# Optimization experiments

Hardware: AMD Instinct MI355X
Metric: run time of the kernel (lower is better)

Reference implementation:

```python
import jax, jax.numpy as jnp
import numpy as np

B, T, C, H = 2, 2048, 1024, 16
D = C // H  # head_dim = 64

def setup_inputs() -> dict:
    key = jax.random.key(0)
    ks = jax.random.split(key, 9)
    s = 1.0 / np.sqrt(C)
    return {
        "x": jax.random.normal(ks[0], (B, T, C), dtype=jnp.float32),
        "Wq": jax.random.uniform(ks[1], (C, C), jnp.float32, -s, s),
        "bq": jax.random.uniform(ks[2], (C,), jnp.float32, -s, s),
        "Wk": jax.random.uniform(ks[3], (C, C), jnp.float32, -s, s),
        "bk": jax.random.uniform(ks[4], (C,), jnp.float32, -s, s),
        "Wv": jax.random.uniform(ks[5], (C, C), jnp.float32, -s, s),
        "bv": jax.random.uniform(ks[6], (C,), jnp.float32, -s, s),
        "Wp": jax.random.uniform(ks[7], (C, C), jnp.float32, -s, s),
        "bp": jax.random.uniform(ks[8], (C,), jnp.float32, -s, s),
    }

def reference(x, Wq, bq, Wk, bk, Wv, bv, Wp, bp):
    # Linear layers: torch nn.Linear weight is [out,in], so x @ W.T + b
    q = x @ Wq.T + bq
    k = x @ Wk.T + bk
    v = x @ Wv.T + bv
    # [B,T,C] -> [B,H,T,D]
    q = q.reshape(B, T, H, D).transpose(0, 2, 1, 3)
    k = k.reshape(B, T, H, D).transpose(0, 2, 1, 3)
    v = v.reshape(B, T, H, D).transpose(0, 2, 1, 3)
    att = jnp.einsum("bhqd,bhkd->bhqk", q, k) / jnp.sqrt(jnp.float32(D))
    causal = jnp.tril(jnp.ones((T, T), dtype=bool))  # [T,T]
    att = jnp.where(causal, att, jnp.float32(-jnp.inf))
    att = jax.nn.softmax(att, axis=-1)
    out = jnp.einsum("bhqk,bhkd->bhqd", att, v)
    out = out.transpose(0, 2, 1, 3).reshape(B, T, C)
    return out @ Wp.T + bp
```

## Files before the change

kernel.cpp:

```cpp
#include <hip/hip_runtime.h>
#include <hip/hip_bf16.h>
#include <stdint.h>

typedef __bf16 bf16x8 __attribute__((ext_vector_type(8)));
typedef __bf16 bf16x4 __attribute__((ext_vector_type(4)));
typedef __bf16 bf16x2 __attribute__((ext_vector_type(2)));
typedef float  f32x4  __attribute__((ext_vector_type(4)));
typedef float  f32x16v __attribute__((ext_vector_type(16)));

#define MFMA16(A,B,Cc) __builtin_amdgcn_mfma_f32_16x16x32_bf16(A,B,Cc,0,0,0)
#define MFMA32(A,B,Cc) __builtin_amdgcn_mfma_f32_32x32x16_bf16(A,B,Cc,0,0,0)

__device__ inline unsigned pack2(float a, float b) {
  union { bf16x2 v; unsigned u; } t;
  t.v[0] = (__bf16)a; t.v[1] = (__bf16)b;
  return t.u;
}
__device__ inline bf16x8 frag4(unsigned w0, unsigned w1, unsigned w2, unsigned w3) {
  union { unsigned u[4]; bf16x8 v; } t;
  t.u[0] = w0; t.u[1] = w1; t.u[2] = w2; t.u[3] = w3;
  return t.v;
}

__device__ inline void pswap(unsigned& a, unsigned& b) {
#if __has_builtin(__builtin_amdgcn_permlane32_swap)
  auto r = __builtin_amdgcn_permlane32_swap(a, b, false, false);
  a = r[0]; b = r[1];
#else
  asm volatile("v_permlane32_swap_b32 %0, %1" : "+v"(a), "+v"(b));
#endif
}
__device__ inline float cross32_max(float v) {
  unsigned a = __builtin_bit_cast(unsigned, v), b = a;
  pswap(a, b);
  return fmaxf(__builtin_bit_cast(float, a), __builtin_bit_cast(float, b));
}
__device__ inline float cross32_sum(float v) {
  unsigned a = __builtin_bit_cast(unsigned, v), b = a;
  pswap(a, b);
  return __builtin_bit_cast(float, a) + __builtin_bit_cast(float, b);
}

__device__ inline void gl16(const __bf16* g, __bf16* l) {
  __builtin_amdgcn_global_load_lds(
      (const __attribute__((address_space(1))) void*)(uintptr_t)g,
      (__attribute__((address_space(3))) void*)(uintptr_t)l, 16, 0, 0);
}

__global__ __launch_bounds__(256) void conv_kernel(
    const float* __restrict__ x,
    const float* __restrict__ Wq, const float* __restrict__ Wk,
    const float* __restrict__ Wv, const float* __restrict__ Wp,
    __bf16* __restrict__ xb, __bf16* __restrict__ Wb)
{
  const int z = blockIdx.y;
  const float* src;
  __bf16* dst;
  int n4;
  if (z == 0) { src = x;  dst = xb; n4 = 1048576; }
  else {
    src = (z == 1) ? Wq : (z == 2) ? Wk : (z == 3) ? Wv : Wp;
    dst = Wb + (size_t)(z - 1) * 1048576;
    n4  = 262144;
  }
  const f32x4* s4 = (const f32x4*)src;
  for (int i = blockIdx.x * 256 + threadIdx.x; i < n4; i += gridDim.x * 256) {
    const f32x4 v = s4[i];
    bf16x4 o;
#pragma unroll
    for (int j = 0; j < 4; ++j) o[j] = (__bf16)v[j];
    *(bf16x4*)(dst + (size_t)i * 4) = o;
  }
}

__device__ inline void gemm_core(const __bf16* __restrict__ A,
                                 const __bf16* __restrict__ W,
                                 int m0, int n0,
                                 __bf16* As, __bf16* Bs,
                                 f32x4 (&acc)[4][4])
{
  const int tid = threadIdx.x, lane = tid & 63;
  const int wid = tid >> 6, wr = wid >> 1, wc = wid & 1;
  const int g = lane >> 4, cl = lane & 15;
  const int sr = tid >> 2, sk = (tid & 3) * 8;
  __bf16* AsW = As + (tid & 192) * 8;
  __bf16* BsW = Bs + (tid & 192) * 8;

  for (int k0 = 0; k0 < 1024; k0 += 32) {
    __syncthreads();
    gl16(A + (size_t)(m0 + sr)      * 1024 + k0 + sk, AsW);
    gl16(A + (size_t)(m0 + sr + 64) * 1024 + k0 + sk, AsW + 2048);
    gl16(W + (size_t)(n0 + sr)      * 1024 + k0 + sk, BsW);
    gl16(W + (size_t)(n0 + sr + 64) * 1024 + k0 + sk, BsW + 2048);
    __syncthreads();
    bf16x8 af[4], bfr[4];
#pragma unroll
    for (int m = 0; m < 4; ++m)
      af[m] = *(const bf16x8*)(As + (wr * 64 + m * 16 + cl) * 32 + g * 8);
#pragma unroll
    for (int n = 0; n < 4; ++n)
      bfr[n] = *(const bf16x8*)(Bs + (wc * 64 + n * 16 + cl) * 32 + g * 8);
#pragma unroll
    for (int m = 0; m < 4; ++m)
#pragma unroll
      for (int n = 0; n < 4; ++n)
        acc[m][n] = MFMA16(af[m], bfr[n], acc[m][n]);
  }
}

__global__ __launch_bounds__(256) void gemm_qkv128(
    const __bf16* __restrict__ xb, const __bf16* __restrict__ Wb,
    const float* __restrict__ bq, const float* __restrict__ bk,
    const float* __restrict__ bv,
    __bf16* __restrict__ Qw, __bf16* __restrict__ Kw, __bf16* __restrict__ Vw)
{
  __shared__ __align__(16) __bf16 As[128 * 32];
  __shared__ __align__(16) __bf16 Bs[128 * 32];

  const int orig = blockIdx.x;
  const int wg   = (orig & 7) * 96 + (orig >> 3);
  const int z    = wg >> 8;
  const int rem  = wg & 255;
  const int m0   = (rem >> 3) * 128;
  const int n0   = (rem & 7) * 128;

  const __bf16* W  = Wb + (size_t)z * 1048576;
  const float*  bi = (z == 0) ? bq : (z == 1) ? bk : bv;
  __bf16*       out = (z == 0) ? Qw : (z == 1) ? Kw : Vw;

  f32x4 acc[4][4] = {};
  gemm_core(xb, W, m0, n0, As, Bs, acc);

  const int lane = threadIdx.x & 63, wid = threadIdx.x >> 6;
  const int wr = wid >> 1, wc = wid & 1;
  const int g = lane >> 4, cl = lane & 15;

  float bvv[4];
#pragma unroll
  for (int n = 0; n < 4; ++n) bvv[n] = bi[n0 + wc * 64 + n * 16 + cl];

#pragma unroll
  for (int m = 0; m < 4; ++m)
#pragma unroll
    for (int n = 0; n < 4; ++n) {
      const int col = n0 + wc * 64 + n * 16 + cl;
      const int h = col >> 6, d = col & 63;
      if (z == 2) {
        const int row0 = m0 + wr * 64 + m * 16 + g * 4;
        const int b2 = row0 >> 11, t0 = row0 & 2047;
        bf16x4 v4;
#pragma unroll
        for (int j = 0; j < 4; ++j) v4[j] = (__bf16)(acc[m][n][j] + bvv[n]);
        *(bf16x4*)(out + (size_t)(b2 * 16 + h) * 131072 + (size_t)d * 2048 + t0) = v4;
      } else {
#pragma unroll
        for (int j = 0; j < 4; ++j) {
          const int row = m0 + wr * 64 + m * 16 + g * 4 + j;
          const int b2 = row >> 11, t = row & 2047;
          out[(size_t)(b2 * 16 + h) * 131072 + (size_t)t * 64 + d] =
              (__bf16)(acc[m][n][j] + bvv[n]);
        }
      }
    }
}

__global__ __launch_bounds__(256) void gemm_proj128(
    const __bf16* __restrict__ A, const __bf16* __restrict__ W,
    const float* __restrict__ bi, float* __restrict__ outp)
{
  __shared__ __align__(16) __bf16 As[128 * 32];
  __shared__ __align__(16) __bf16 Bs[128 * 32];

  const int orig = blockIdx.x;
  const int wg   = (orig & 7) * 32 + (orig >> 3);
  const int m0   = (wg >> 3) * 128;
  const int n0   = (wg & 7) * 128;

  f32x4 acc[4][4] = {};
  gemm_core(A, W, m0, n0, As, Bs, acc);

  const int lane = threadIdx.x & 63, wid = threadIdx.x >> 6;
  const int wr = wid >> 1, wc = wid & 1;
  const int g = lane >> 4, cl = lane & 15;

  float bvv[4];
#pragma unroll
  for (int n = 0; n < 4; ++n) bvv[n] = bi[n0 + wc * 64 + n * 16 + cl];
#pragma unroll
  for (int m = 0; m < 4; ++m)
#pragma unroll
    for (int n = 0; n < 4; ++n) {
      const int col = n0 + wc * 64 + n * 16 + cl;
#pragma unroll
      for (int j = 0; j < 4; ++j) {
        const int row = m0 + wr * 64 + m * 16 + g * 4 + j;
        outp[(size_t)row * 1024 + col] = acc[m][n][j] + bvv[n];
      }
    }
}

__device__ inline void attn_tile(
    const __bf16* __restrict__ Kb, const __bf16* __restrict__ vrow0,
    const __bf16* __restrict__ vrow1, const bf16x8 (&qf)[4],
    int kv0, bool diag, int l31, int hi,
    float& M, float& MS, float& L, f32x16v& o0, f32x16v& o1)
{
  const float SC = 0.18033688f;
  const float DT = 16.6f;

  const bf16x8 kf0 = *(const bf16x8*)(Kb + (kv0 + l31) * 64 +      hi * 8);
  const bf16x8 kf1 = *(const bf16x8*)(Kb + (kv0 + l31) * 64 + 16 + hi * 8);
  const bf16x8 kf2 = *(const bf16x8*)(Kb + (kv0 + l31) * 64 + 32 + hi * 8);
  const bf16x8 kf3 = *(const bf16x8*)(Kb + (kv0 + l31) * 64 + 48 + hi * 8);
  const bf16x8 va0 = *(const bf16x8*)(vrow0 + kv0 + hi * 8);
  const bf16x8 va1 = *(const bf16x8*)(vrow1 + kv0 + hi * 8);
  const bf16x8 va2 = *(const bf16x8*)(vrow0 + kv0 + 16 + hi * 8);
  const bf16x8 va3 = *(const bf16x8*)(vrow1 + kv0 + 16 + hi * 8);

  f32x16v s = {};
  s = MFMA32(kf0, qf[0], s);
  s = MFMA32(kf1, qf[1], s);
  s = MFMA32(kf2, qf[2], s);
  s = MFMA32(kf3, qf[3], s);

  if (diag) {
#pragma unroll
    for (int r = 0; r < 16; ++r) {
      const int kl = (r & 3) + 8 * (r >> 2) + 4 * hi;
      if (kl > l31) s[r] = -1e30f;
    }
  }
  float mt = fmaxf(s[0], s[1]);
#pragma unroll
  for (int r = 2; r < 16; ++r) mt = fmaxf(mt, s[r]);
  mt = cross32_max(mt);
  if (!__all(mt <= M + DT)) {
    const float Mn = fmaxf(M, mt);
    const float rs = exp2f((M - Mn) * SC);
    o0 *= rs; o1 *= rs; L *= rs; M = Mn; MS = M * SC;
  }
  float pr[16];
  float lt = 0.f;
#pragma unroll
  for (int r = 0; r < 16; ++r) {
    pr[r] = exp2f(__builtin_fmaf(s[r], SC, -MS));
    lt += pr[r];
  }
  L += cross32_sum(lt);

  unsigned c0 = pack2(pr[0],  pr[1]),  c1 = pack2(pr[2],  pr[3]);
  unsigned c2 = pack2(pr[4],  pr[5]),  c3 = pack2(pr[6],  pr[7]);
  unsigned c4 = pack2(pr[8],  pr[9]),  c5 = pack2(pr[10], pr[11]);
  unsigned c6 = pack2(pr[12], pr[13]), c7 = pack2(pr[14], pr[15]);
  pswap(c0, c2);
  pswap(c1, c3);
  pswap(c4, c6);
  pswap(c5, c7);
  const bf16x8 pf0 = frag4(c0, c1, c2, c3);
  const bf16x8 pf1 = frag4(c4, c5, c6, c7);

  o0 = MFMA32(va0, pf0, o0);
  o1 = MFMA32(va1, pf0, o1);
  o0 = MFMA32(va2, pf1, o0);
  o1 = MFMA32(va3, pf1, o1);
}

__global__ __launch_bounds__(256, 4) void attn_kernel(
    const __bf16* __restrict__ Q, const __bf16* __restrict__ K,
    const __bf16* __restrict__ Vt, __bf16* __restrict__ Oc)
{
  const int bh  = blockIdx.x;
  const int p   = blockIdx.y;
  const int w   = threadIdx.x >> 6;
  const int lane = threadIdx.x & 63;
  const int l31 = lane & 31, hi = lane >> 5;
  const float SC = 0.18033688f;

  const __bf16* Qb = Q  + (size_t)bh * 131072;
  const __bf16* Kb = K  + (size_t)bh * 131072;
  const __bf16* Vb = Vt + (size_t)bh * 131072;
  const __bf16* vrow0 = Vb + (size_t)l31 * 2048;
  const __bf16* vrow1 = Vb + (size_t)(32 + l31) * 2048;

  __shared__ __bf16 SO[8][64][36];
  __shared__ float  SML[8][64][2];

  const int qsS[2] = { p * 32, (63 - p) * 32 };
  const int nS[2]  = { p + 1, 64 - p };

#pragma unroll
  for (int ph = 0; ph < 2; ++ph) {
    const int qs = qsS[ph], nT = nS[ph];
    bf16x8 qf[4];
#pragma unroll
    for (int c = 0; c < 4; ++c)
      qf[c] = *(const bf16x8*)(Qb + (qs + l31) * 64 + c * 16 + hi * 8);

    f32x16v o0 = {}, o1 = {};
    float M = -1e30f, L = 0.f;
    float MS = M * SC;

    for (int t = w; t < nT; t += 4)
      attn_tile(Kb, vrow0, vrow1, qf, t * 32, t == nT - 1, l31, hi,
                M, MS, L, o0, o1);

    const int slot = ph * 4 + w;
#pragma unroll
    for (int q4 = 0; q4 < 4; ++q4) {
      bf16x4 a, b;
#pragma unroll
      for (int j = 0; j < 4; ++j) {
        a[j] = (__bf16)o0[q4 * 4 + j];
        b[j] = (__bf16)o1[q4 * 4 + j];
      }
      *(bf16x4*)&SO[slot][lane][q4 * 4]      = a;
      *(bf16x4*)&SO[slot][lane][16 + q4 * 4] = b;
    }
    SML[slot][lane][0] = M;
    SML[slot][lane][1] = L;
  }

  __syncthreads();
  if (w < 2) {
    const int base = w * 4;
    const int qs = qsS[w];
    float Mw[4], Lw[4];
#pragma unroll
    for (int s = 0; s < 4; ++s) {
      Mw[s] = SML[base + s][lane][0];
      Lw[s] = SML[base + s][lane][1];
    }
    const float Ms = fmaxf(fmaxf(Mw[0], Mw[1]), fmaxf(Mw[2], Mw[3]));
    float r[4], Lt = 0.f;
#pragma unroll
    for (int s = 0; s < 4; ++s) {
      r[s] = exp2f((Mw[s] - Ms) * SC);
      Lt += Lw[s] * r[s];
    }
    const float inv = 1.0f / Lt;

    const int b = bh >> 4, h = bh & 15;
    const int tq = qs + l31;
    __bf16* orow = Oc + (size_t)(b * 2048 + tq) * 1024 + h * 64;
#pragma unroll
    for (int q4 = 0; q4 < 4; ++q4) {
      bf16x4 v0, v1;
      float acc0[4] = {}, acc1[4] = {};
#pragma unroll
      for (int s = 0; s < 4; ++s) {
        const bf16x4 a4 = *(const bf16x4*)&SO[base + s][lane][q4 * 4];
        const bf16x4 b4 = *(const bf16x4*)&SO[base + s][lane][16 + q4 * 4];
#pragma unroll
        for (int j = 0; j < 4; ++j) {
          acc0[j] += (float)a4[j] * r[s];
          acc1[j] += (float)b4[j] * r[s];
        }
      }
#pragma unroll
      for (int j = 0; j < 4; ++j) {
        v0[j] = (__bf16)(acc0[j] * inv);
        v1[j] = (__bf16)(acc1[j] * inv);
      }
      const int d0 = 8 * q4 + 4 * hi;
      *(bf16x4*)(orow + d0)      = v0;
      *(bf16x4*)(orow + 32 + d0) = v1;
    }
  }
}

extern "C" void kernel_launch(void* const* d_in, const int* in_sizes, int n_in,
                              void* d_out, int out_size, void* d_ws, size_t ws_size,
                              hipStream_t stream) {
  const float* x  = (const float*)d_in[0];
  const float* Wq = (const float*)d_in[1];
  const float* bq = (const float*)d_in[2];
  const float* Wk = (const float*)d_in[3];
  const float* bk = (const float*)d_in[4];
  const float* Wv = (const float*)d_in[5];
  const float* bv = (const float*)d_in[6];
  const float* Wp = (const float*)d_in[7];
  const float* bp = (const float*)d_in[8];

  __bf16* Qw  = (__bf16*)d_ws;
  __bf16* Kw  = Qw + (size_t)4194304;
  __bf16* Vw  = Kw + (size_t)4194304;
  __bf16* xbA = Vw + (size_t)4194304;
  __bf16* Wb  = xbA + (size_t)4194304;

  conv_kernel<<<dim3(512, 5), 256, 0, stream>>>(x, Wq, Wk, Wv, Wp, xbA, Wb);
  gemm_qkv128<<<768, 256, 0, stream>>>(xbA, Wb, bq, bk, bv, Qw, Kw, Vw);
  attn_kernel<<<dim3(32, 32), 256, 0, stream>>>(Qw, Kw, Vw, xbA );
  gemm_proj128<<<256, 256, 0, stream>>>(xbA , Wb + (size_t)3 * 1048576,
                                        bp, (float*)d_out);
}
```

Before: 134.3 us.

## Split causal attention over KV halves with partial outputs and a merge kernel

Adds a split-KV attention path. Each workgroup handles a paired short/long query tile with half of the KV tiles across 4 waves, writes bf16 partial outputs plus max/sum to workspace, and a separate merge kernel combines the two halves and writes the final head-interleaved output. The goal is more parallelism and better balance across the causal triangle (2048 smaller blocks at higher occupancy). The cost is an extra launch, workspace traffic for the partials, and extra bf16 rounding of those partials. The new path is used only when the workspace is large enough; otherwise the old kernel runs.

```diff
diff --git a/kernel.cpp b/kernel.cpp
--- a/kernel.cpp
+++ b/kernel.cpp
@@ -265,7 +265,154 @@
   o1 = MFMA32(va3, pf1, o1);
 }
 
-__global__ __launch_bounds__(256, 4) void attn_kernel(
+__global__ __launch_bounds__(256, 8) void attn_part(
+    const __bf16* __restrict__ Q, const __bf16* __restrict__ K,
+    const __bf16* __restrict__ Vt, __bf16* __restrict__ PO,
+    float* __restrict__ PML)
+{
+  const int lin  = blockIdx.x;
+  const int wg   = (lin & 7) * 256 + (lin >> 3);
+  const int bh   = wg >> 6;
+  const int rem  = wg & 63;
+  const int pair = rem >> 1, half = rem & 1;
+  const int w    = threadIdx.x >> 6;
+  const int lane = threadIdx.x & 63;
+  const int l31 = lane & 31, hi = lane >> 5;
+  const float SC = 0.18033688f;
+
+  __shared__ __bf16 SO[4][64][36];
+  __shared__ float  SML[4][64][2];
+
+  const __bf16* Qb = Q  + (size_t)bh * 131072;
+  const __bf16* Kb = K  + (size_t)bh * 131072;
+  const __bf16* Vb = Vt + (size_t)bh * 131072;
+  const __bf16* vrow0 = Vb + (size_t)l31 * 2048;
+  const __bf16* vrow1 = Vb + (size_t)(32 + l31) * 2048;
+
+  const int qsS[2] = { pair * 32, (63 - pair) * 32 };
+  const int nS[2]  = { pair + 1, 64 - pair };
+
+  for (int ph = 0; ph < 2; ++ph) {
+    const int qs = qsS[ph], nT = nS[ph];
+    bf16x8 qf[4];
+#pragma unroll
+    for (int c = 0; c < 4; ++c)
+      qf[c] = *(const bf16x8*)(Qb + (qs + l31) * 64 + c * 16 + hi * 8);
+
+    f32x16v o0 = {}, o1 = {};
+    float M = -1e30f, L = 0.f;
+    float MS = M * SC;
+
+    for (int t = 4 * half + w; t < nT; t += 8)
+      attn_tile(Kb, vrow0, vrow1, qf, t * 32, t == nT - 1, l31, hi,
+                M, MS, L, o0, o1);
+
+#pragma unroll
+    for (int q4 = 0; q4 < 4; ++q4) {
+      bf16x4 a, b;
+#pragma unroll
+      for (int j = 0; j < 4; ++j) {
+        a[j] = (__bf16)o0[q4 * 4 + j];
+        b[j] = (__bf16)o1[q4 * 4 + j];
+      }
+      *(bf16x4*)&SO[w][lane][q4 * 4]      = a;
+      *(bf16x4*)&SO[w][lane][16 + q4 * 4] = b;
+    }
+    SML[w][lane][0] = M;
+    SML[w][lane][1] = L;
+    __syncthreads();
+
+    {
+      float Mw[4], Lw[4];
+#pragma unroll
+      for (int s = 0; s < 4; ++s) {
+        Mw[s] = SML[s][lane][0];
+        Lw[s] = SML[s][lane][1];
+      }
+      const float Ms = fmaxf(fmaxf(Mw[0], Mw[1]), fmaxf(Mw[2], Mw[3]));
+      float r[4], Lt = 0.f;
+#pragma unroll
+      for (int s = 0; s < 4; ++s) {
+        r[s] = exp2f((Mw[s] - Ms) * SC);
+        Lt += Lw[s] * r[s];
+      }
+      float acc[8] = {};
+#pragma unroll
+      for (int s = 0; s < 4; ++s) {
+        const bf16x4 A0 = *(const bf16x4*)&SO[s][lane][w * 8];
+        const bf16x4 A1 = *(const bf16x4*)&SO[s][lane][w * 8 + 4];
+#pragma unroll
+        for (int j = 0; j < 4; ++j) {
+          acc[j]     += (float)A0[j] * r[s];
+          acc[4 + j] += (float)A1[j] * r[s];
+        }
+      }
+      const size_t slot = ((((size_t)bh * 32 + pair) * 2 + half) * 2 + ph);
+      bf16x8 v;
+#pragma unroll
+      for (int j = 0; j < 8; ++j) v[j] = (__bf16)acc[j];
+      *(bf16x8*)(PO + slot * 2048 + lane * 32 + w * 8) = v;
+      if (w == 0) {
+        PML[slot * 128 + lane * 2]     = Ms;
+        PML[slot * 128 + lane * 2 + 1] = Lt;
+      }
+    }
+    __syncthreads();
+  }
+}
+
+__global__ __launch_bounds__(256, 8) void attn_merge(
+    const __bf16* __restrict__ PO, const float* __restrict__ PML,
+    __bf16* __restrict__ Oc)
+{
+  const int task = blockIdx.x * 4 + (threadIdx.x >> 6);
+  const int bh = task >> 6, s = task & 63;
+  const int lane = threadIdx.x & 63;
+  const int l31 = lane & 31, hi = lane >> 5;
+  const float SC = 0.18033688f;
+
+  const int p  = (s < 32) ? s : 63 - s;
+  const int ph = (s < 32) ? 0 : 1;
+  const size_t s0 = ((((size_t)bh * 32 + p) * 2 + 0) * 2 + ph);
+  const size_t s1 = ((((size_t)bh * 32 + p) * 2 + 1) * 2 + ph);
+
+  const float M0 = PML[s0 * 128 + lane * 2], L0 = PML[s0 * 128 + lane * 2 + 1];
+  const float M1 = PML[s1 * 128 + lane * 2], L1 = PML[s1 * 128 + lane * 2 + 1];
+  const float Ms = fmaxf(M0, M1);
+  const float r0 = exp2f((M0 - Ms) * SC);
+  const float r1 = exp2f((M1 - Ms) * SC);
+  const float inv = 1.0f / (L0 * r0 + L1 * r1);
+
+  const __bf16* p0 = PO + s0 * 2048 + lane * 32;
+  const __bf16* p1 = PO + s1 * 2048 + lane * 32;
+  float out[32];
+#pragma unroll
+  for (int q = 0; q < 4; ++q) {
+    const bf16x8 a = *(const bf16x8*)(p0 + q * 8);
+    const bf16x8 b = *(const bf16x8*)(p1 + q * 8);
+#pragma unroll
+    for (int j = 0; j < 8; ++j)
+      out[q * 8 + j] = ((float)a[j] * r0 + (float)b[j] * r1) * inv;
+  }
+
+  const int b = bh >> 4, h = bh & 15;
+  const int t = s * 32 + l31;
+  __bf16* orow = Oc + (size_t)(b * 2048 + t) * 1024 + h * 64;
+#pragma unroll
+  for (int rg = 0; rg < 4; ++rg) {
+    const int d0 = rg * 8 + 4 * hi;
+    bf16x4 v0, v1;
+#pragma unroll
+    for (int j = 0; j < 4; ++j) {
+      v0[j] = (__bf16)out[rg * 4 + j];
+      v1[j] = (__bf16)out[16 + rg * 4 + j];
+    }
+    *(bf16x4*)(orow + d0)      = v0;
+    *(bf16x4*)(orow + 32 + d0) = v1;
+  }
+}
+
+__global__ __launch_bounds__(256, 4) void attn_kernel_lds(
     const __bf16* __restrict__ Q, const __bf16* __restrict__ K,
     const __bf16* __restrict__ Vt, __bf16* __restrict__ Oc)
 {
@@ -381,15 +528,26 @@
   const float* Wp = (const float*)d_in[7];
   const float* bp = (const float*)d_in[8];
 
-  __bf16* Qw  = (__bf16*)d_ws;
-  __bf16* Kw  = Qw + (size_t)4194304;
-  __bf16* Vw  = Kw + (size_t)4194304;
-  __bf16* xbA = Vw + (size_t)4194304;
-  __bf16* Wb  = xbA + (size_t)4194304;
-
-  conv_kernel<<<dim3(512, 5), 256, 0, stream>>>(x, Wq, Wk, Wv, Wp, xbA, Wb);
-  gemm_qkv128<<<768, 256, 0, stream>>>(xbA, Wb, bq, bk, bv, Qw, Kw, Vw);
-  attn_kernel<<<dim3(32, 32), 256, 0, stream>>>(Qw, Kw, Vw, xbA );
-  gemm_proj128<<<256, 256, 0, stream>>>(xbA , Wb + (size_t)3 * 1048576,
+  __bf16* base = (__bf16*)d_ws;
+  __bf16* Qw = base;
+  __bf16* Kw = base + (size_t)4194304;
+  __bf16* Vw = base + (size_t)8388608;
+  __bf16* Wb = base + (size_t)12582912;
+  __bf16* Aw = base + (size_t)16777216;
+  __bf16* PO = base + (size_t)20971520;
+  float*  PML = (float*)((char*)d_ws + 58720256);
+
+  const bool big = ws_size >= (size_t)60817408;
+  __bf16* xb = big ? PO : Aw;
+
+  conv_kernel<<<dim3(512, 5), 256, 0, stream>>>(x, Wq, Wk, Wv, Wp, xb, Wb);
+  gemm_qkv128<<<768, 256, 0, stream>>>(xb, Wb, bq, bk, bv, Qw, Kw, Vw);
+  if (big) {
+    attn_part<<<2048, 256, 0, stream>>>(Qw, Kw, Vw, PO, PML);
+    attn_merge<<<512, 256, 0, stream>>>(PO, PML, Aw);
+  } else {
+    attn_kernel_lds<<<dim3(32, 32), 256, 0, stream>>>(Qw, Kw, Vw, Aw);
+  }
+  gemm_proj128<<<256, 256, 0, stream>>>(Aw, Wb + (size_t)3 * 1048576,
                                         bp, (float*)d_out);
 }
```

After: 331.0 us. 146% more time.
